# Kernel optimization log

Hardware: AMD Instinct MI355X
Metric: run time of the kernel (lower is better)

## Reference

```python
import jax, jax.numpy as jnp
import numpy as np

D = 1024   # model dim
H = 16     # heads
HD = D // H
L = 14     # layers
FF = 4096  # ffn hidden
T = 768    # sequence length


def layer_norm(x, g, b, eps):
    m = x.mean(-1, keepdims=True)
    v = ((x - m) ** 2).mean(-1, keepdims=True)
    return (x - m) / jnp.sqrt(v + eps) * g + b


def rel_pos_emb(t, d):
    # EspnetRelPositionalEncoding: concat(flip(pe_positive), pe_negative[1:]) -> (1, 2t-1, d)
    pos = jnp.arange(t, dtype=jnp.float32)
    div = jnp.exp(jnp.arange(0, d, 2, dtype=jnp.float32) * (-jnp.log(10000.0) / d))
    ang = pos[:, None] * div[None, :]                              # (t, d/2)
    pe_pos = jnp.stack([jnp.sin(ang), jnp.cos(ang)], -1).reshape(t, d)
    pe_neg = jnp.stack([jnp.sin(-ang), jnp.cos(-ang)], -1).reshape(t, d)
    return jnp.concatenate([pe_pos[::-1], pe_neg[1:]], 0)[None]    # (1, 2t-1, d)


def rel_shift(x):
    # x: (b, h, t, 2t-1) -> (b, h, t, t), Transformer-XL shift
    b, h, t, n = x.shape
    xp = jnp.concatenate([jnp.zeros((b, h, t, 1), x.dtype), x], -1)  # (b,h,t,n+1)
    xp = xp.reshape(b, h, n + 1, t)
    x = xp[:, :, 1:].reshape(b, h, t, n)
    return x[..., : n // 2 + 1]


def setup_inputs() -> dict:
    key = jax.random.key(0)
    ks = iter(jax.random.split(key, 40))
    s = 0.02
    nrm = lambda k, shape: jax.random.normal(k, shape, dtype=jnp.float32) * s
    return {
        "xs": jax.random.normal(next(ks), (1, T, D), dtype=jnp.float32),
        "embed_W": nrm(next(ks), (D, D)), "embed_b": jnp.zeros((D,), jnp.float32),
        "embed_ln_g": jnp.ones((D,), jnp.float32), "embed_ln_b": jnp.zeros((D,), jnp.float32),
        "Wq": nrm(next(ks), (L, D, D)), "bq": jnp.zeros((L, D), jnp.float32),
        "Wk": nrm(next(ks), (L, D, D)), "bk": jnp.zeros((L, D), jnp.float32),
        "Wv": nrm(next(ks), (L, D, D)), "bv": jnp.zeros((L, D), jnp.float32),
        "Wo": nrm(next(ks), (L, D, D)), "bo": jnp.zeros((L, D), jnp.float32),
        "Wp": nrm(next(ks), (L, D, D)),
        "pos_u": nrm(next(ks), (L, H, HD)), "pos_v": nrm(next(ks), (L, H, HD)),
        "ln1_g": jnp.ones((L, D), jnp.float32), "ln1_b": jnp.zeros((L, D), jnp.float32),
        "ln2_g": jnp.ones((L, D), jnp.float32), "ln2_b": jnp.zeros((L, D), jnp.float32),
        "ff_W1": nrm(next(ks), (L, D, FF)), "ff_b1": jnp.zeros((L, FF), jnp.float32),
        "ff_W2": nrm(next(ks), (L, FF, D)), "ff_b2": jnp.zeros((L, D), jnp.float32),
        "after_g": jnp.ones((D,), jnp.float32), "after_b": jnp.zeros((D,), jnp.float32),
    }


def reference(xs, embed_W, embed_b, embed_ln_g, embed_ln_b,
              Wq, bq, Wk, bk, Wv, bv, Wo, bo, Wp, pos_u, pos_v,
              ln1_g, ln1_b, ln2_g, ln2_b, ff_W1, ff_b1, ff_W2, ff_b2,
              after_g, after_b):
    b, t, _ = xs.shape
    # LegacyLinearNoSubsampling: Linear -> LayerNorm(eps=1e-5) -> (dropout) -> ReLU
    h = jnp.maximum(layer_norm(xs @ embed_W + embed_b, embed_ln_g, embed_ln_b, 1e-5), 0.0)
    x = h * jnp.sqrt(jnp.float32(D))          # pos-enc scale factor
    pos = rel_pos_emb(t, D)                    # (1, 2t-1, D)
    scale = jnp.float32(HD) ** -0.5
    for i in range(L):
        res = x
        xn = layer_norm(x, ln1_g[i], ln1_b[i], 1e-12)
        q = (xn @ Wq[i] + bq[i]).reshape(b, t, H, HD).transpose(0, 2, 1, 3)   # bhtd
        k = (xn @ Wk[i] + bk[i]).reshape(b, t, H, HD).transpose(0, 2, 1, 3)
        v = (xn @ Wv[i] + bv[i]).reshape(b, t, H, HD).transpose(0, 2, 1, 3)
        p = (pos @ Wp[i]).reshape(1, 2 * t - 1, H, HD).transpose(0, 2, 1, 3)  # bhnd
        ac = jnp.einsum('bhtd,bhsd->bhts', q + pos_u[i][None, :, None, :], k)
        bd = rel_shift(jnp.einsum('bhtd,bhnd->bhtn', q + pos_v[i][None, :, None, :], p))
        attn = jax.nn.softmax((ac + bd) * scale, axis=-1)
        o = jnp.einsum('bhts,bhsd->bhtd', attn, v).transpose(0, 2, 1, 3).reshape(b, t, D)
        x = res + (o @ Wo[i] + bo[i])
        res = x
        xn = layer_norm(x, ln2_g[i], ln2_b[i], 1e-12)
        x = res + (jnp.maximum(xn @ ff_W1[i] + ff_b1[i], 0.0) @ ff_W2[i] + ff_b2[i])
    return layer_norm(x, after_g, after_b, 1e-5)
```

## Files before the change

### kernel.cpp

```cpp
#include <hip/hip_runtime.h>
#include <hip/hip_bf16.h>
#include <math.h>

#define D_    1024
#define H_    16
#define HD_   64
#define L_    14
#define FF_   4096
#define T_    768
#define NPOS_ (2*T_-1)

using s16x8 = __attribute__((ext_vector_type(8))) short;
using f32x4 = __attribute__((ext_vector_type(4))) float;

__device__ inline short f2bf(float f) {
  __hip_bfloat16 h = __float2bfloat16(f);
  return *reinterpret_cast<short*>(&h);
}
__device__ inline float bf2f(unsigned short u) {
  union { unsigned u; float f; } v; v.u = ((unsigned)u) << 16; return v.f;
}

__device__ inline float waveRedSum(float v) {
#pragma unroll
  for (int o = 32; o > 0; o >>= 1) v += __shfl_down(v, o, 64);
  return v;
}
__device__ inline float blockRedSum(float v, float* sh) {
  int lane = threadIdx.x & 63, wid = threadIdx.x >> 6;
  v = waveRedSum(v);
  if (lane == 0) sh[wid] = v;
  __syncthreads();
  if (wid == 0) {
    float x = (lane < 4) ? sh[lane] : 0.f;
    x = waveRedSum(x);
    if (lane == 0) sh[0] = x;
  }
  __syncthreads();
  float r = sh[0];
  __syncthreads();
  return r;
}

__global__ __launch_bounds__(256) void ln_kernel(
    const float* __restrict__ x, const float* __restrict__ g,
    const float* __restrict__ b, void* __restrict__ y,
    float eps, int relu, float scale, int obf)
{
  __shared__ float sh[8];
  long row = blockIdx.x;
  const float* xr = x + row * D_;
  int tid = threadIdx.x;
  float4 v = *(const float4*)&xr[tid * 4];
  float s  = v.x + v.y + v.z + v.w;
  float sq = v.x * v.x + v.y * v.y + v.z * v.z + v.w * v.w;
  float mean = blockRedSum(s, sh) * (1.f / D_);
  float esq  = blockRedSum(sq, sh) * (1.f / D_);
  float var  = esq - mean * mean;
  if (var < 0.f) var = 0.f;
  float inv = rsqrtf(var + eps);
  float4 gv = *(const float4*)&g[tid * 4];
  float4 bv = *(const float4*)&b[tid * 4];
  float o0 = (v.x - mean) * inv * gv.x + bv.x;
  float o1 = (v.y - mean) * inv * gv.y + bv.y;
  float o2 = (v.z - mean) * inv * gv.z + bv.z;
  float o3 = (v.w - mean) * inv * gv.w + bv.w;
  if (relu) {
    o0 = fmaxf(o0, 0.f); o1 = fmaxf(o1, 0.f);
    o2 = fmaxf(o2, 0.f); o3 = fmaxf(o3, 0.f);
  }
  o0 *= scale; o1 *= scale; o2 *= scale; o3 *= scale;
  if (obf) {
    short4 sv;
    sv.x = f2bf(o0); sv.y = f2bf(o1); sv.z = f2bf(o2); sv.w = f2bf(o3);
    *(short4*)&((unsigned short*)y)[row * D_ + tid * 4] = sv;
  } else {
    float4 ov; ov.x = o0; ov.y = o1; ov.z = o2; ov.w = o3;
    *(float4*)&((float*)y)[row * D_ + tid * 4] = ov;
  }
}

__global__ __launch_bounds__(256) void transpose_kernel(
    const float* __restrict__ in, unsigned short* __restrict__ out, int K, int N)
{
  __shared__ unsigned short t[32][33];
  long z = blockIdx.z;
  in  += z * (long)K * N;
  out += z * (long)K * N;
  int n0 = blockIdx.x * 32, k0 = blockIdx.y * 32;
  int tid = threadIdx.x;
  int r = tid >> 3, c4 = (tid & 7) * 4;
  float4 v = *(const float4*)&in[(long)(k0 + r) * N + n0 + c4];
  t[r][c4 + 0] = (unsigned short)f2bf(v.x);
  t[r][c4 + 1] = (unsigned short)f2bf(v.y);
  t[r][c4 + 2] = (unsigned short)f2bf(v.z);
  t[r][c4 + 3] = (unsigned short)f2bf(v.w);
  __syncthreads();
  ushort4 s;
  s.x = t[c4 + 0][r]; s.y = t[c4 + 1][r]; s.z = t[c4 + 2][r]; s.w = t[c4 + 3][r];
  *(ushort4*)&out[(long)(n0 + r) * K + k0 + c4] = s;
}

template<int BM, int BN, int BMODE, bool CBF16>
__global__ __launch_bounds__(256) void gemm4_kernel(
    const unsigned short* __restrict__ A, int lda, long sAz,
    const void* __restrict__ B0, const void* __restrict__ B1, const void* __restrict__ B2,
    int ldb, long sBz,
    void* C0, void* C1, void* C2, int ldc, long sCz,
    const float* __restrict__ bias0, const float* __restrict__ bias1,
    const float* __restrict__ bias2,
    const float* __restrict__ resid, int ldres,
    int M, int N, int K, int zPerG, int relu, int nM)
{
  constexpr int FM = BM / 32, FN = BN / 32;
  constexpr int A_IT = BM / 32;
  constexpr int NSH = (BN == 128) ? 7 : 6;

  __shared__ short As[BM * 64];
  __shared__ short Bs[BN * 64];

  int nb = gridDim.x, bid = blockIdx.x;
  int q = nb >> 3, r = nb & 7, xcd = bid & 7, idx = bid >> 3;
  int lbid = (xcd < r ? xcd * (q + 1) : r * (q + 1) + (xcd - r) * q) + idx;
  int mT = lbid % nM, nT = lbid / nM;
  int m0 = mT * BM, n0 = nT * BN;

  int z = blockIdx.z;
  int g = z / zPerG, zb = z - g * zPerG;
  A += (long)zb * sAz;
  const void* Bv = (g == 0) ? B0 : ((g == 1) ? B1 : B2);
  void* Cv       = (g == 0) ? C0 : ((g == 1) ? C1 : C2);
  const float* bias = (g == 0) ? bias0 : ((g == 1) ? bias1 : bias2);
  const float* Bf = (const float*)Bv + zb * sBz;
  const unsigned short* Bh = (const unsigned short*)Bv + zb * sBz;
  float* Cf = (float*)Cv + zb * sCz;
  unsigned short* Ch = (unsigned short*)Cv + zb * sCz;

  int tid = threadIdx.x, lane = tid & 63, wid = tid >> 6;
  int wm0 = (wid >> 1) * (BM / 2), wn0 = (wid & 1) * (BN / 2);
  int lr = lane & 15, kl = (lane >> 4) * 8;

  f32x4 acc[FM][FN];
#pragma unroll
  for (int i = 0; i < FM; ++i)
#pragma unroll
    for (int j = 0; j < FN; ++j)
#pragma unroll
      for (int rr = 0; rr < 4; ++rr) acc[i][j][rr] = 0.f;

  for (int k0 = 0; k0 < K; k0 += 64) {
#pragma unroll
    for (int it = 0; it < A_IT; ++it) {
      int f = tid + it * 256;
      int row = f >> 3, c8 = f & 7;
      int gm = m0 + row;
      s16x8 v = {0, 0, 0, 0, 0, 0, 0, 0};
      if (gm < M) v = *(const s16x8*)(A + (long)gm * lda + k0 + c8 * 8);
      *(s16x8*)&As[row * 64 + ((c8 ^ (row & 7)) << 3)] = v;
    }
    if constexpr (BMODE == 1) {
      constexpr int B_IT = BN / 32;
#pragma unroll
      for (int it = 0; it < B_IT; ++it) {
        int f = tid + it * 256;
        int row = f >> 3, c8 = f & 7;
        int gn = n0 + row;
        s16x8 v = *(const s16x8*)(Bh + (long)gn * ldb + k0 + c8 * 8);
        *(s16x8*)&Bs[row * 64 + ((c8 ^ (row & 7)) << 3)] = v;
      }
    } else {
      constexpr int B_IT = BN / 16;
#pragma unroll
      for (int it = 0; it < B_IT; ++it) {
        int p = tid + it * 256;
        int n = p & (BN - 1), kq = p >> NSH;
        int gn = n0 + n;
        const float* bp = Bf + (long)(k0 + kq * 4) * ldb + gn;
        short4 s;
        s.x = f2bf(bp[0]); s.y = f2bf(bp[ldb]);
        s.z = f2bf(bp[2 * (long)ldb]); s.w = f2bf(bp[3 * (long)ldb]);
        *(short4*)&Bs[n * 64 + ((kq << 2) ^ ((n & 7) << 3))] = s;
      }
    }
    __syncthreads();
#pragma unroll
    for (int kk = 0; kk < 2; ++kk) {
      s16x8 a[FM], b[FN];
#pragma unroll
      for (int i = 0; i < FM; ++i) {
        int row = wm0 + i * 16 + lr;
        a[i] = *(const s16x8*)&As[row * 64 + ((kk * 32 + kl) ^ ((lr & 7) << 3))];
      }
#pragma unroll
      for (int j = 0; j < FN; ++j) {
        int row = wn0 + j * 16 + lr;
        b[j] = *(const s16x8*)&Bs[row * 64 + ((kk * 32 + kl) ^ ((lr & 7) << 3))];
      }
#pragma unroll
      for (int i = 0; i < FM; ++i)
#pragma unroll
        for (int j = 0; j < FN; ++j)
          acc[i][j] = __builtin_amdgcn_mfma_f32_16x16x32_bf16(a[i], b[j], acc[i][j], 0, 0, 0);
    }
    __syncthreads();
  }
#pragma unroll
  for (int i = 0; i < FM; ++i) {
#pragma unroll
    for (int j = 0; j < FN; ++j) {
      int n = n0 + wn0 + j * 16 + lr;
      float bv = bias ? bias[n] : 0.f;
#pragma unroll
      for (int rr = 0; rr < 4; ++rr) {
        int m = m0 + wm0 + i * 16 + (lane >> 4) * 4 + rr;
        if (m < M) {
          float v = acc[i][j][rr] + bv;
          if (resid) v += resid[(long)m * ldres + n];
          if (relu)  v = fmaxf(v, 0.f);
          if constexpr (CBF16) Ch[(long)m * ldc + n] = (unsigned short)f2bf(v);
          else                 Cf[(long)m * ldc + n] = v;
        }
      }
    }
  }
}

__global__ __launch_bounds__(256) void f2bf_kernel(
    const float* __restrict__ x, unsigned short* __restrict__ y, int n4)
{
  int i = blockIdx.x * 256 + threadIdx.x;
  if (i >= n4) return;
  float4 v = *(const float4*)&x[i * 4];
  short4 s; s.x = f2bf(v.x); s.y = f2bf(v.y); s.z = f2bf(v.z); s.w = f2bf(v.w);
  *(short4*)&y[i * 4] = s;
}

__global__ __launch_bounds__(256) void pos_kernel(unsigned short* __restrict__ pos)
{
  int idx = blockIdx.x * 256 + threadIdx.x;
  if (idx >= NPOS_ * (D_ / 2)) return;
  int n = idx / (D_ / 2), i = idx % (D_ / 2);
  float r = (float)(T_ - 1 - n);
  float div = __expf((float)(2 * i) * (-logf(10000.f) / (float)D_));
  float ang = r * div;
  pos[(long)n * D_ + 2 * i]     = (unsigned short)f2bf(sinf(ang));
  pos[(long)n * D_ + 2 * i + 1] = (unsigned short)f2bf(cosf(ang));
}

__global__ __launch_bounds__(256) void flash_attn_kernel(
    const unsigned short* __restrict__ Q, const unsigned short* __restrict__ K,
    const unsigned short* __restrict__ V, const unsigned short* __restrict__ P,
    const float* __restrict__ posu, const float* __restrict__ posv,
    unsigned short* __restrict__ O)
{
  __shared__ short Ks[64 * 64];
  __shared__ short Vs[64 * 64];
  __shared__ short Ps[96 * 64];
  __shared__ float Grgn[32 * 99];
  __shared__ float mxls[2][32], smls[2][32];

  short* qu = (short*)Grgn;
  short* qv = qu + 32 * 64;
  float* G  = Grgn;
  short* Pf = (short*)Grgn;

  int h = blockIdx.y;
  int t0 = blockIdx.x * 32;
  int tid = threadIdx.x, lane = tid & 63, w = tid >> 6;
  int wr = w >> 1, wc = w & 1;
  int lr = lane & 15, lg = lane >> 4;
  int kl = lg * 8;
  const float* pu = posu + h * HD_;
  const float* pv = posv + h * HD_;

  {
    int row = tid >> 3, c8 = tid & 7;
    s16x8 q8 = *(const s16x8*)(Q + (long)(t0 + row) * D_ + h * HD_ + c8 * 8);
    const unsigned short* qp = (const unsigned short*)&q8;
    s16x8 su, sv;
#pragma unroll
    for (int j = 0; j < 8; ++j) {
      float qf = bf2f(qp[j]);
      su[j] = f2bf(qf + pu[c8 * 8 + j]);
      sv[j] = f2bf(qf + pv[c8 * 8 + j]);
    }
    int sw = row * 64 + ((c8 ^ (row & 7)) << 3);
    *(s16x8*)&qu[sw] = su;
    *(s16x8*)&qv[sw] = sv;
  }
  __syncthreads();
  s16x8 aqu[2], aqv[2];
#pragma unroll
  for (int kk = 0; kk < 2; ++kk) {
    int row = wr * 16 + lr;
    int col = (kk * 32 + kl) ^ ((lr & 7) << 3);
    aqu[kk] = *(const s16x8*)&qu[row * 64 + col];
    aqv[kk] = *(const s16x8*)&qv[row * 64 + col];
  }

  float m_[4], l_[4];
  f32x4 acc_o[2];
#pragma unroll
  for (int rr = 0; rr < 4; ++rr) { m_[rr] = -1e30f; l_[rr] = 0.f; }
#pragma unroll
  for (int j = 0; j < 2; ++j)
#pragma unroll
    for (int rr = 0; rr < 4; ++rr) acc_o[j][rr] = 0.f;

  for (int s0 = 0; s0 < T_; s0 += 64) {
    int base = s0 - t0 + T_ - 32;
    __syncthreads();
#pragma unroll
    for (int it = 0; it < 2; ++it) {
      int f = tid + it * 256;
      int row = f >> 3, c8 = f & 7;
      s16x8 v = *(const s16x8*)(K + (long)(s0 + row) * D_ + h * HD_ + c8 * 8);
      *(s16x8*)&Ks[row * 64 + ((c8 ^ (row & 7)) << 3)] = v;
    }
#pragma unroll
    for (int it = 0; it < 4; ++it) {
      int d = tid & 63, sq = tid >> 6;
      int s = it * 16 + sq * 4;
      const unsigned short* vp = V + (long)(s0 + s) * D_ + h * HD_ + d;
      short4 sv4;
      sv4.x = (short)vp[0];
      sv4.y = (short)vp[D_];
      sv4.z = (short)vp[2 * D_];
      sv4.w = (short)vp[3 * D_];
      *(short4*)&Vs[d * 64 + (s ^ ((d & 7) << 3))] = sv4;
    }
#pragma unroll
    for (int it = 0; it < 3; ++it) {
      int f = tid + it * 256;
      int row = f >> 3, c8 = f & 7;
      int gp = base + row; if (gp > NPOS_ - 1) gp = NPOS_ - 1;
      s16x8 v = *(const s16x8*)(P + (long)gp * D_ + h * HD_ + c8 * 8);
      *(s16x8*)&Ps[row * 64 + ((c8 ^ (row & 7)) << 3)] = v;
    }
    __syncthreads();
    f32x4 a_ac[2], a_g[3];
#pragma unroll
    for (int j = 0; j < 2; ++j)
#pragma unroll
      for (int rr = 0; rr < 4; ++rr) a_ac[j][rr] = 0.f;
#pragma unroll
    for (int j = 0; j < 3; ++j)
#pragma unroll
      for (int rr = 0; rr < 4; ++rr) a_g[j][rr] = 0.f;
#pragma unroll
    for (int j = 0; j < 2; ++j)
#pragma unroll
      for (int kk = 0; kk < 2; ++kk) {
        int row = wc * 32 + j * 16 + lr;
        s16x8 b = *(const s16x8*)&Ks[row * 64 + ((kk * 32 + kl) ^ ((lr & 7) << 3))];
        a_ac[j] = __builtin_amdgcn_mfma_f32_16x16x32_bf16(aqu[kk], b, a_ac[j], 0, 0, 0);
      }
#pragma unroll
    for (int j = 0; j < 3; ++j)
#pragma unroll
      for (int kk = 0; kk < 2; ++kk) {
        int row = wc * 48 + j * 16 + lr;
        s16x8 b = *(const s16x8*)&Ps[row * 64 + ((kk * 32 + kl) ^ ((lr & 7) << 3))];
        a_g[j] = __builtin_amdgcn_mfma_f32_16x16x32_bf16(aqv[kk], b, a_g[j], 0, 0, 0);
      }
#pragma unroll
    for (int j = 0; j < 3; ++j)
#pragma unroll
      for (int rr = 0; rr < 4; ++rr) {
        int row = wr * 16 + lg * 4 + rr;
        int col = wc * 48 + j * 16 + lr;
        G[row * 99 + col] = a_g[j][rr];
      }
    __syncthreads();
    float sreg[2][4], pm[4];
#pragma unroll
    for (int rr = 0; rr < 4; ++rr) {
      int row = wr * 16 + lg * 4 + rr;
#pragma unroll
      for (int j = 0; j < 2; ++j) {
        int c = wc * 32 + j * 16 + lr;
        int gc = c - row + 31;
        sreg[j][rr] = (a_ac[j][rr] + G[row * 99 + gc]) * 0.125f;
      }
      pm[rr] = fmaxf(sreg[0][rr], sreg[1][rr]);
    }
#pragma unroll
    for (int o = 1; o < 16; o <<= 1)
#pragma unroll
      for (int rr = 0; rr < 4; ++rr) pm[rr] = fmaxf(pm[rr], __shfl_xor(pm[rr], o, 64));
    if (lr == 0) {
#pragma unroll
      for (int rr = 0; rr < 4; ++rr) mxls[wc][wr * 16 + lg * 4 + rr] = pm[rr];
    }
    __syncthreads();
    float ps[4];
#pragma unroll
    for (int rr = 0; rr < 4; ++rr) {
      int row = wr * 16 + lg * 4 + rr;
      float mnew = fmaxf(m_[rr], fmaxf(mxls[0][row], mxls[1][row]));
      float sc = __expf(m_[rr] - mnew);
      m_[rr] = mnew;
      l_[rr] *= sc;
      acc_o[0][rr] *= sc;
      acc_o[1][rr] *= sc;
      float p0 = __expf(sreg[0][rr] - mnew);
      float p1 = __expf(sreg[1][rr] - mnew);
      ps[rr] = p0 + p1;
      int c0 = wc * 32 + lr, c1 = wc * 32 + 16 + lr;
      ((unsigned short*)Pf)[row * 64 + (c0 ^ ((row & 7) << 3))] = (unsigned short)f2bf(p0);
      ((unsigned short*)Pf)[row * 64 + (c1 ^ ((row & 7) << 3))] = (unsigned short)f2bf(p1);
    }
#pragma unroll
    for (int o = 1; o < 16; o <<= 1)
#pragma unroll
      for (int rr = 0; rr < 4; ++rr) ps[rr] += __shfl_xor(ps[rr], o, 64);
    if (lr == 0) {
#pragma unroll
      for (int rr = 0; rr < 4; ++rr) smls[wc][wr * 16 + lg * 4 + rr] = ps[rr];
    }
    __syncthreads();
#pragma unroll
    for (int rr = 0; rr < 4; ++rr) {
      int row = wr * 16 + lg * 4 + rr;
      l_[rr] += smls[0][row] + smls[1][row];
    }
    s16x8 ap[2];
#pragma unroll
    for (int kk = 0; kk < 2; ++kk) {
      int row = wr * 16 + lr;
      ap[kk] = *(const s16x8*)&((unsigned short*)Pf)[row * 64 + ((kk * 32 + kl) ^ ((lr & 7) << 3))];
    }
#pragma unroll
    for (int j = 0; j < 2; ++j)
#pragma unroll
      for (int kk = 0; kk < 2; ++kk) {
        int row = wc * 32 + j * 16 + lr;
        s16x8 b = *(const s16x8*)&Vs[row * 64 + ((kk * 32 + kl) ^ ((lr & 7) << 3))];
        acc_o[j] = __builtin_amdgcn_mfma_f32_16x16x32_bf16(ap[kk], b, acc_o[j], 0, 0, 0);
      }
  }
#pragma unroll
  for (int j = 0; j < 2; ++j)
#pragma unroll
    for (int rr = 0; rr < 4; ++rr) {
      int row = t0 + wr * 16 + lg * 4 + rr;
      int col = h * HD_ + wc * 32 + j * 16 + lr;
      O[(long)row * D_ + col] = (unsigned short)f2bf(acc_o[j][rr] / l_[rr]);
    }
}

extern "C" void kernel_launch(void* const* d_in, const int* in_sizes, int n_in,
                              void* d_out, int out_size, void* d_ws, size_t ws_size,
                              hipStream_t stream) {
  const float* xs       = (const float*)d_in[0];
  const float* embed_W  = (const float*)d_in[1];
  const float* embed_b  = (const float*)d_in[2];
  const float* embed_g  = (const float*)d_in[3];
  const float* embed_bt = (const float*)d_in[4];
  const float* Wq = (const float*)d_in[5];
  const float* bq = (const float*)d_in[6];
  const float* Wk = (const float*)d_in[7];
  const float* bk = (const float*)d_in[8];
  const float* Wv = (const float*)d_in[9];
  const float* bv = (const float*)d_in[10];
  const float* Wo = (const float*)d_in[11];
  const float* bo = (const float*)d_in[12];
  const float* Wp = (const float*)d_in[13];
  const float* pos_u = (const float*)d_in[14];
  const float* pos_v = (const float*)d_in[15];
  const float* ln1_g = (const float*)d_in[16];
  const float* ln1_b = (const float*)d_in[17];
  const float* ln2_g = (const float*)d_in[18];
  const float* ln2_b = (const float*)d_in[19];
  const float* ff_W1 = (const float*)d_in[20];
  const float* ff_b1 = (const float*)d_in[21];
  const float* ff_W2 = (const float*)d_in[22];
  const float* ff_b2 = (const float*)d_in[23];
  const float* after_g = (const float*)d_in[24];
  const float* after_b = (const float*)d_in[25];
  float* out = (float*)d_out;

  char* w = (char*)d_ws;
  auto carve = [&](size_t bytes) { char* p = w; w += (bytes + 255) & ~(size_t)255; return p; };
  float* bufX  = (float*)carve((size_t)T_ * D_ * 4);
  float* bufT  = (float*)carve((size_t)T_ * D_ * 4);
  unsigned short* xsb  = (unsigned short*)carve((size_t)T_ * D_ * 2);
  unsigned short* XNb  = (unsigned short*)carve((size_t)T_ * D_ * 2);
  unsigned short* Qb   = (unsigned short*)carve((size_t)T_ * D_ * 2);
  unsigned short* Kb   = (unsigned short*)carve((size_t)T_ * D_ * 2);
  unsigned short* Vb   = (unsigned short*)carve((size_t)T_ * D_ * 2);
  unsigned short* Ob   = (unsigned short*)carve((size_t)T_ * D_ * 2);
  unsigned short* Hb   = (unsigned short*)carve((size_t)T_ * FF_ * 2);
  unsigned short* posT = (unsigned short*)carve((size_t)NPOS_ * D_ * 2);
  unsigned short* Pall = (unsigned short*)carve((size_t)L_ * NPOS_ * D_ * 2);
  size_t szDD = (size_t)D_ * D_;
  unsigned short* embedWt = (unsigned short*)carve(szDD * 2);
  unsigned short* WqT = (unsigned short*)carve((size_t)L_ * szDD * 2);
  unsigned short* WkT = (unsigned short*)carve((size_t)L_ * szDD * 2);
  unsigned short* WvT = (unsigned short*)carve((size_t)L_ * szDD * 2);
  unsigned short* WoT = (unsigned short*)carve((size_t)L_ * szDD * 2);
  unsigned short* WpT = (unsigned short*)carve((size_t)L_ * szDD * 2);
  unsigned short* W1T = (unsigned short*)carve((size_t)L_ * D_ * FF_ * 2);
  unsigned short* W2T = (unsigned short*)carve((size_t)L_ * D_ * FF_ * 2);
  bool fast = ((size_t)(w - (char*)d_ws) <= ws_size);

  {
    int n = NPOS_ * (D_ / 2);
    pos_kernel<<<(n + 255) / 256, 256, 0, stream>>>(posT);
  }
  f2bf_kernel<<<(T_ * D_ / 4 + 255) / 256, 256, 0, stream>>>(xs, xsb, T_ * D_ / 4);

  if (fast) {
    transpose_kernel<<<dim3(32, 32, 1),  256, 0, stream>>>(embed_W, embedWt, D_, D_);
    transpose_kernel<<<dim3(32, 32, L_), 256, 0, stream>>>(Wq, WqT, D_, D_);
    transpose_kernel<<<dim3(32, 32, L_), 256, 0, stream>>>(Wk, WkT, D_, D_);
    transpose_kernel<<<dim3(32, 32, L_), 256, 0, stream>>>(Wv, WvT, D_, D_);
    transpose_kernel<<<dim3(32, 32, L_), 256, 0, stream>>>(Wo, WoT, D_, D_);
    transpose_kernel<<<dim3(32, 32, L_), 256, 0, stream>>>(Wp, WpT, D_, D_);
    transpose_kernel<<<dim3(128, 32, L_), 256, 0, stream>>>(ff_W1, W1T, D_, FF_);
    transpose_kernel<<<dim3(32, 128, L_), 256, 0, stream>>>(ff_W2, W2T, FF_, D_);

    gemm4_kernel<32, 128, 1, false><<<dim3(192, 1, 1), 256, 0, stream>>>(
        xsb, D_, 0, embedWt, nullptr, nullptr, D_, 0,
        bufT, nullptr, nullptr, D_, 0, embed_b, nullptr, nullptr,
        nullptr, 0, T_, D_, D_, 1, 0, 24);
    ln_kernel<<<T_, 256, 0, stream>>>(bufT, embed_g, embed_bt, bufX, 1e-5f, 1, 32.0f, 0);

    gemm4_kernel<128, 64, 1, true><<<dim3(192, 1, 14), 256, 0, stream>>>(
        posT, D_, 0, WpT, nullptr, nullptr, D_, (long)szDD,
        Pall, nullptr, nullptr, D_, (long)NPOS_ * D_, nullptr, nullptr, nullptr,
        nullptr, 0, NPOS_, D_, D_, 14, 0, 12);

    for (int i = 0; i < L_; ++i) {
      ln_kernel<<<T_, 256, 0, stream>>>(bufX, ln1_g + (long)i * D_, ln1_b + (long)i * D_,
                                        XNb, 1e-12f, 0, 1.0f, 1);
      gemm4_kernel<32, 128, 1, true><<<dim3(192, 1, 3), 256, 0, stream>>>(
          XNb, D_, 0, WqT + i * szDD, WkT + i * szDD, WvT + i * szDD, D_, 0,
          Qb, Kb, Vb, D_, 0,
          bq + (long)i * D_, bk + (long)i * D_, bv + (long)i * D_,
          nullptr, 0, T_, D_, D_, 1, 0, 24);
      flash_attn_kernel<<<dim3(T_ / 32, H_), 256, 0, stream>>>(
          Qb, Kb, Vb, Pall + (long)i * NPOS_ * D_,
          pos_u + (long)i * D_, pos_v + (long)i * D_, Ob);
      gemm4_kernel<32, 64, 1, false><<<dim3(384, 1, 1), 256, 0, stream>>>(
          Ob, D_, 0, WoT + i * szDD, nullptr, nullptr, D_, 0,
          bufX, nullptr, nullptr, D_, 0, bo + (long)i * D_, nullptr, nullptr,
          bufX, D_, T_, D_, D_, 1, 0, 24);
      ln_kernel<<<T_, 256, 0, stream>>>(bufX, ln2_g + (long)i * D_, ln2_b + (long)i * D_,
                                        XNb, 1e-12f, 0, 1.0f, 1);
      gemm4_kernel<32, 128, 1, true><<<dim3(768, 1, 1), 256, 0, stream>>>(
          XNb, D_, 0, W1T + (size_t)i * D_ * FF_, nullptr, nullptr, D_, 0,
          Hb, nullptr, nullptr, FF_, 0, ff_b1 + (long)i * FF_, nullptr, nullptr,
          nullptr, 0, T_, FF_, D_, 1, 1, 24);
      gemm4_kernel<32, 64, 1, false><<<dim3(384, 1, 1), 256, 0, stream>>>(
          Hb, FF_, 0, W2T + (size_t)i * D_ * FF_, nullptr, nullptr, FF_, 0,
          bufX, nullptr, nullptr, D_, 0, ff_b2 + (long)i * D_, nullptr, nullptr,
          bufX, D_, T_, FF_, FF_, 1, 0, 24);
    }
  } else {
    gemm4_kernel<32, 128, 0, false><<<dim3(192, 1, 1), 256, 0, stream>>>(
        xsb, D_, 0, embed_W, nullptr, nullptr, D_, 0,
        bufT, nullptr, nullptr, D_, 0, embed_b, nullptr, nullptr,
        nullptr, 0, T_, D_, D_, 1, 0, 24);
    ln_kernel<<<T_, 256, 0, stream>>>(bufT, embed_g, embed_bt, bufX, 1e-5f, 1, 32.0f, 0);

    gemm4_kernel<128, 64, 0, true><<<dim3(192, 1, 14), 256, 0, stream>>>(
        posT, D_, 0, Wp, nullptr, nullptr, D_, (long)szDD,
        Pall, nullptr, nullptr, D_, (long)NPOS_ * D_, nullptr, nullptr, nullptr,
        nullptr, 0, NPOS_, D_, D_, 14, 0, 12);

    for (int i = 0; i < L_; ++i) {
      ln_kernel<<<T_, 256, 0, stream>>>(bufX, ln1_g + (long)i * D_, ln1_b + (long)i * D_,
                                        XNb, 1e-12f, 0, 1.0f, 1);
      gemm4_kernel<32, 128, 0, true><<<dim3(192, 1, 3), 256, 0, stream>>>(
          XNb, D_, 0, Wq + i * szDD, Wk + i * szDD, Wv + i * szDD, D_, 0,
          Qb, Kb, Vb, D_, 0,
          bq + (long)i * D_, bk + (long)i * D_, bv + (long)i * D_,
          nullptr, 0, T_, D_, D_, 1, 0, 24);
      flash_attn_kernel<<<dim3(T_ / 32, H_), 256, 0, stream>>>(
          Qb, Kb, Vb, Pall + (long)i * NPOS_ * D_,
          pos_u + (long)i * D_, pos_v + (long)i * D_, Ob);
      gemm4_kernel<32, 64, 0, false><<<dim3(384, 1, 1), 256, 0, stream>>>(
          Ob, D_, 0, Wo + i * szDD, nullptr, nullptr, D_, 0,
          bufX, nullptr, nullptr, D_, 0, bo + (long)i * D_, nullptr, nullptr,
          bufX, D_, T_, D_, D_, 1, 0, 24);
      ln_kernel<<<T_, 256, 0, stream>>>(bufX, ln2_g + (long)i * D_, ln2_b + (long)i * D_,
                                        XNb, 1e-12f, 0, 1.0f, 1);
      gemm4_kernel<32, 128, 0, true><<<dim3(768, 1, 1), 256, 0, stream>>>(
          XNb, D_, 0, ff_W1 + (size_t)i * D_ * FF_, nullptr, nullptr, FF_, 0,
          Hb, nullptr, nullptr, FF_, 0, ff_b1 + (long)i * FF_, nullptr, nullptr,
          nullptr, 0, T_, FF_, D_, 1, 1, 24);
      gemm4_kernel<32, 64, 0, false><<<dim3(384, 1, 1), 256, 0, stream>>>(
          Hb, FF_, 0, ff_W2 + (size_t)i * D_ * FF_, nullptr, nullptr, D_, 0,
          bufX, nullptr, nullptr, D_, 0, ff_b2 + (long)i * D_, nullptr, nullptr,
          bufX, D_, T_, FF_, FF_, 1, 0, 24);
    }
  }

  ln_kernel<<<T_, 256, 0, stream>>>(bufX, after_g, after_b, out, 1e-5f, 0, 1.0f, 0);
}
```

Baseline: 2.501 ms.

## Add 32x32x16 MFMA GEMM kernel with configurable wave layout for fast path

After: 3.029 ms. 1.21x slower.

```diff
diff --git a/kernel.cpp b/kernel.cpp
--- a/kernel.cpp
+++ b/kernel.cpp
@@ -10,8 +10,9 @@
 #define T_    768
 #define NPOS_ (2*T_-1)
 
-using s16x8 = __attribute__((ext_vector_type(8))) short;
-using f32x4 = __attribute__((ext_vector_type(4))) float;
+using s16x8  = __attribute__((ext_vector_type(8))) short;
+using f32x4  = __attribute__((ext_vector_type(4))) float;
+using f32x16 = __attribute__((ext_vector_type(16))) float;
 
 __device__ inline short f2bf(float f) {
   __hip_bfloat16 h = __float2bfloat16(f);
@@ -101,8 +102,103 @@
   *(ushort4*)&out[(long)(n0 + r) * K + k0 + c4] = s;
 }
 
-template<int BM, int BN, int BMODE, bool CBF16>
-__global__ __launch_bounds__(256) void gemm4_kernel(
+template<int BM, int BN, int WM, int WN, bool CBF16>
+__global__ __launch_bounds__(WM * WN * 64) void gemm7_kernel(
+    const unsigned short* __restrict__ A, int lda, long sAz,
+    const unsigned short* __restrict__ B0, const unsigned short* __restrict__ B1,
+    const unsigned short* __restrict__ B2, int ldb, long sBz,
+    void* C0, void* C1, void* C2, int ldc, long sCz,
+    const float* __restrict__ bias0, const float* __restrict__ bias1,
+    const float* __restrict__ bias2,
+    const float* __restrict__ resid, int ldres,
+    int M, int N, int K, int zPerG, int relu, int nM)
+{
+  constexpr int NT = WM * WN * 64;
+  constexpr int FM = BM / WM / 32;
+  constexpr int A_IT = BM * 8 / NT;
+  constexpr int B_IT = BN * 8 / NT;
+
+  __shared__ short As[BM * 64];
+  __shared__ short Bs[BN * 64];
+
+  int nb = gridDim.x, bid = blockIdx.x;
+  int q = nb >> 3, r = nb & 7, xcd = bid & 7, idx = bid >> 3;
+  int lbid = (xcd < r ? xcd * (q + 1) : r * (q + 1) + (xcd - r) * q) + idx;
+  int mT = lbid % nM, nT = lbid / nM;
+  int m0 = mT * BM, n0 = nT * BN;
+
+  int z = blockIdx.z;
+  int g = z / zPerG, zb = z - g * zPerG;
+  A += (long)zb * sAz;
+  const unsigned short* Bh = ((g == 0) ? B0 : ((g == 1) ? B1 : B2)) + zb * sBz;
+  void* Cv = (g == 0) ? C0 : ((g == 1) ? C1 : C2);
+  const float* bias = (g == 0) ? bias0 : ((g == 1) ? bias1 : bias2);
+  float* Cf = (float*)Cv + zb * sCz;
+  unsigned short* Ch = (unsigned short*)Cv + zb * sCz;
+
+  int tid = threadIdx.x, lane = tid & 63, wid = tid >> 6;
+  int wrow = wid / WN, wcol = wid % WN;
+  int wm0 = wrow * (BM / WM), wn0 = wcol * 32;
+  int l31 = lane & 31, khalf = lane >> 5;
+
+  f32x16 acc[FM];
+#pragma unroll
+  for (int i = 0; i < FM; ++i)
+#pragma unroll
+    for (int rr = 0; rr < 16; ++rr) acc[i][rr] = 0.f;
+
+  for (int k0 = 0; k0 < K; k0 += 64) {
+#pragma unroll
+    for (int it = 0; it < A_IT; ++it) {
+      int f = tid + it * NT;
+      int row = f >> 3, c8 = f & 7;
+      int gm = m0 + row;
+      s16x8 v = {0, 0, 0, 0, 0, 0, 0, 0};
+      if (gm < M) v = *(const s16x8*)(A + (long)gm * lda + k0 + c8 * 8);
+      *(s16x8*)&As[row * 64 + ((c8 ^ (row & 7)) << 3)] = v;
+    }
+#pragma unroll
+    for (int it = 0; it < B_IT; ++it) {
+      int f = tid + it * NT;
+      int row = f >> 3, c8 = f & 7;
+      s16x8 v = *(const s16x8*)(Bh + (long)(n0 + row) * ldb + k0 + c8 * 8);
+      *(s16x8*)&Bs[row * 64 + ((c8 ^ (row & 7)) << 3)] = v;
+    }
+    __syncthreads();
+#pragma unroll
+    for (int ks = 0; ks < 4; ++ks) {
+      int c8 = ks * 2 + khalf;
+      int nrow = wn0 + l31;
+      s16x8 b = *(const s16x8*)&Bs[nrow * 64 + ((c8 ^ (nrow & 7)) << 3)];
+#pragma unroll
+      for (int i = 0; i < FM; ++i) {
+        int mrow = wm0 + i * 32 + l31;
+        s16x8 a = *(const s16x8*)&As[mrow * 64 + ((c8 ^ (mrow & 7)) << 3)];
+        acc[i] = __builtin_amdgcn_mfma_f32_32x32x16_bf16(a, b, acc[i], 0, 0, 0);
+      }
+    }
+    __syncthreads();
+  }
+  int n = n0 + wn0 + l31;
+  float bv = bias ? bias[n] : 0.f;
+#pragma unroll
+  for (int i = 0; i < FM; ++i) {
+#pragma unroll
+    for (int reg = 0; reg < 16; ++reg) {
+      int m = m0 + wm0 + i * 32 + (reg & 3) + 8 * (reg >> 2) + 4 * khalf;
+      if (m < M) {
+        float v = acc[i][reg] + bv;
+        if (resid) v += resid[(long)m * ldres + n];
+        if (relu)  v = fmaxf(v, 0.f);
+        if constexpr (CBF16) Ch[(long)m * ldc + n] = (unsigned short)f2bf(v);
+        else                 Cf[(long)m * ldc + n] = v;
+      }
+    }
+  }
+}
+
+template<int BM, int BN, bool CBF16>
+__global__ __launch_bounds__(256) void gemm5_kernel(
     const unsigned short* __restrict__ A, int lda, long sAz,
     const void* __restrict__ B0, const void* __restrict__ B1, const void* __restrict__ B2,
     int ldb, long sBz,
@@ -132,7 +228,6 @@
   void* Cv       = (g == 0) ? C0 : ((g == 1) ? C1 : C2);
   const float* bias = (g == 0) ? bias0 : ((g == 1) ? bias1 : bias2);
   const float* Bf = (const float*)Bv + zb * sBz;
-  const unsigned short* Bh = (const unsigned short*)Bv + zb * sBz;
   float* Cf = (float*)Cv + zb * sCz;
   unsigned short* Ch = (unsigned short*)Cv + zb * sCz;
 
@@ -158,29 +253,17 @@
       if (gm < M) v = *(const s16x8*)(A + (long)gm * lda + k0 + c8 * 8);
       *(s16x8*)&As[row * 64 + ((c8 ^ (row & 7)) << 3)] = v;
     }
-    if constexpr (BMODE == 1) {
-      constexpr int B_IT = BN / 32;
-#pragma unroll
-      for (int it = 0; it < B_IT; ++it) {
-        int f = tid + it * 256;
-        int row = f >> 3, c8 = f & 7;
-        int gn = n0 + row;
-        s16x8 v = *(const s16x8*)(Bh + (long)gn * ldb + k0 + c8 * 8);
-        *(s16x8*)&Bs[row * 64 + ((c8 ^ (row & 7)) << 3)] = v;
-      }
-    } else {
-      constexpr int B_IT = BN / 16;
-#pragma unroll
-      for (int it = 0; it < B_IT; ++it) {
-        int p = tid + it * 256;
-        int n = p & (BN - 1), kq = p >> NSH;
-        int gn = n0 + n;
-        const float* bp = Bf + (long)(k0 + kq * 4) * ldb + gn;
-        short4 s;
-        s.x = f2bf(bp[0]); s.y = f2bf(bp[ldb]);
-        s.z = f2bf(bp[2 * (long)ldb]); s.w = f2bf(bp[3 * (long)ldb]);
-        *(short4*)&Bs[n * 64 + ((kq << 2) ^ ((n & 7) << 3))] = s;
-      }
+    constexpr int B_IT2 = BN / 16;
+#pragma unroll
+    for (int it = 0; it < B_IT2; ++it) {
+      int p = tid + it * 256;
+      int n = p & (BN - 1), kq = p >> NSH;
+      int gn = n0 + n;
+      const float* bp = Bf + (long)(k0 + kq * 4) * ldb + gn;
+      short4 s;
+      s.x = f2bf(bp[0]); s.y = f2bf(bp[ldb]);
+      s.z = f2bf(bp[2 * (long)ldb]); s.w = f2bf(bp[3 * (long)ldb]);
+      *(short4*)&Bs[n * 64 + ((kq << 2) ^ ((n & 7) << 3))] = s;
     }
     __syncthreads();
 #pragma unroll
@@ -491,7 +574,7 @@
   unsigned short* Vb   = (unsigned short*)carve((size_t)T_ * D_ * 2);
   unsigned short* Ob   = (unsigned short*)carve((size_t)T_ * D_ * 2);
   unsigned short* Hb   = (unsigned short*)carve((size_t)T_ * FF_ * 2);
-  unsigned short* posT = (unsigned short*)carve((size_t)NPOS_ * D_ * 2);
+  unsigned short* posT = (unsigned short*)carve((size_t)(NPOS_ + 16) * D_ * 2);
   unsigned short* Pall = (unsigned short*)carve((size_t)L_ * NPOS_ * D_ * 2);
   size_t szDD = (size_t)D_ * D_;
   unsigned short* embedWt = (unsigned short*)carve(szDD * 2);
@@ -520,13 +603,13 @@
     transpose_kernel<<<dim3(128, 32, L_), 256, 0, stream>>>(ff_W1, W1T, D_, FF_);
     transpose_kernel<<<dim3(32, 128, L_), 256, 0, stream>>>(ff_W2, W2T, FF_, D_);
 
-    gemm4_kernel<32, 128, 1, false><<<dim3(192, 1, 1), 256, 0, stream>>>(
+    gemm7_kernel<32, 128, 1, 4, false><<<dim3(192, 1, 1), 256, 0, stream>>>(
         xsb, D_, 0, embedWt, nullptr, nullptr, D_, 0,
         bufT, nullptr, nullptr, D_, 0, embed_b, nullptr, nullptr,
         nullptr, 0, T_, D_, D_, 1, 0, 24);
     ln_kernel<<<T_, 256, 0, stream>>>(bufT, embed_g, embed_bt, bufX, 1e-5f, 1, 32.0f, 0);
 
-    gemm4_kernel<128, 64, 1, true><<<dim3(192, 1, 14), 256, 0, stream>>>(
+    gemm7_kernel<128, 64, 2, 2, true><<<dim3(192, 1, 14), 256, 0, stream>>>(
         posT, D_, 0, WpT, nullptr, nullptr, D_, (long)szDD,
         Pall, nullptr, nullptr, D_, (long)NPOS_ * D_, nullptr, nullptr, nullptr,
         nullptr, 0, NPOS_, D_, D_, 14, 0, 12);
@@ -534,7 +617,7 @@
     for (int i = 0; i < L_; ++i) {
       ln_kernel<<<T_, 256, 0, stream>>>(bufX, ln1_g + (long)i * D_, ln1_b + (long)i * D_,
                                         XNb, 1e-12f, 0, 1.0f, 1);
-      gemm4_kernel<32, 128, 1, true><<<dim3(192, 1, 3), 256, 0, stream>>>(
+      gemm7_kernel<32, 128, 1, 4, true><<<dim3(192, 1, 3), 256, 0, stream>>>(
           XNb, D_, 0, WqT + i * szDD, WkT + i * szDD, WvT + i * szDD, D_, 0,
           Qb, Kb, Vb, D_, 0,
           bq + (long)i * D_, bk + (long)i * D_, bv + (long)i * D_,
@@ -542,29 +625,29 @@
       flash_attn_kernel<<<dim3(T_ / 32, H_), 256, 0, stream>>>(
           Qb, Kb, Vb, Pall + (long)i * NPOS_ * D_,
           pos_u + (long)i * D_, pos_v + (long)i * D_, Ob);
-      gemm4_kernel<32, 64, 1, false><<<dim3(384, 1, 1), 256, 0, stream>>>(
+      gemm7_kernel<32, 64, 1, 2, false><<<dim3(384, 1, 1), 128, 0, stream>>>(
           Ob, D_, 0, WoT + i * szDD, nullptr, nullptr, D_, 0,
           bufX, nullptr, nullptr, D_, 0, bo + (long)i * D_, nullptr, nullptr,
           bufX, D_, T_, D_, D_, 1, 0, 24);
       ln_kernel<<<T_, 256, 0, stream>>>(bufX, ln2_g + (long)i * D_, ln2_b + (long)i * D_,
                                         XNb, 1e-12f, 0, 1.0f, 1);
-      gemm4_kernel<32, 128, 1, true><<<dim3(768, 1, 1), 256, 0, stream>>>(
+      gemm7_kernel<32, 128, 1, 4, true><<<dim3(768, 1, 1), 256, 0, stream>>>(
           XNb, D_, 0, W1T + (size_t)i * D_ * FF_, nullptr, nullptr, D_, 0,
           Hb, nullptr, nullptr, FF_, 0, ff_b1 + (long)i * FF_, nullptr, nullptr,
           nullptr, 0, T_, FF_, D_, 1, 1, 24);
-      gemm4_kernel<32, 64, 1, false><<<dim3(384, 1, 1), 256, 0, stream>>>(
+      gemm7_kernel<32, 64, 1, 2, false><<<dim3(384, 1, 1), 128, 0, stream>>>(
           Hb, FF_, 0, W2T + (size_t)i * D_ * FF_, nullptr, nullptr, FF_, 0,
           bufX, nullptr, nullptr, D_, 0, ff_b2 + (long)i * D_, nullptr, nullptr,
           bufX, D_, T_, FF_, FF_, 1, 0, 24);
     }
   } else {
-    gemm4_kernel<32, 128, 0, false><<<dim3(192, 1, 1), 256, 0, stream>>>(
+    gemm5_kernel<32, 128, false><<<dim3(192, 1, 1), 256, 0, stream>>>(
         xsb, D_, 0, embed_W, nullptr, nullptr, D_, 0,
         bufT, nullptr, nullptr, D_, 0, embed_b, nullptr, nullptr,
         nullptr, 0, T_, D_, D_, 1, 0, 24);
     ln_kernel<<<T_, 256, 0, stream>>>(bufT, embed_g, embed_bt, bufX, 1e-5f, 1, 32.0f, 0);
 
-    gemm4_kernel<128, 64, 0, true><<<dim3(192, 1, 14), 256, 0, stream>>>(
+    gemm5_kernel<128, 64, true><<<dim3(192, 1, 14), 256, 0, stream>>>(
         posT, D_, 0, Wp, nullptr, nullptr, D_, (long)szDD,
         Pall, nullptr, nullptr, D_, (long)NPOS_ * D_, nullptr, nullptr, nullptr,
         nullptr, 0, NPOS_, D_, D_, 14, 0, 12);
@@ -572,7 +655,7 @@
     for (int i = 0; i < L_; ++i) {
       ln_kernel<<<T_, 256, 0, stream>>>(bufX, ln1_g + (long)i * D_, ln1_b + (long)i * D_,
                                         XNb, 1e-12f, 0, 1.0f, 1);
-      gemm4_kernel<32, 128, 0, true><<<dim3(192, 1, 3), 256, 0, stream>>>(
+      gemm5_kernel<32, 128, true><<<dim3(192, 1, 3), 256, 0, stream>>>(
           XNb, D_, 0, Wq + i * szDD, Wk + i * szDD, Wv + i * szDD, D_, 0,
           Qb, Kb, Vb, D_, 0,
           bq + (long)i * D_, bk + (long)i * D_, bv + (long)i * D_,
@@ -580,17 +663,17 @@
       flash_attn_kernel<<<dim3(T_ / 32, H_), 256, 0, stream>>>(
           Qb, Kb, Vb, Pall + (long)i * NPOS_ * D_,
           pos_u + (long)i * D_, pos_v + (long)i * D_, Ob);
-      gemm4_kernel<32, 64, 0, false><<<dim3(384, 1, 1), 256, 0, stream>>>(
+      gemm5_kernel<32, 64, false><<<dim3(384, 1, 1), 256, 0, stream>>>(
           Ob, D_, 0, Wo + i * szDD, nullptr, nullptr, D_, 0,
           bufX, nullptr, nullptr, D_, 0, bo + (long)i * D_, nullptr, nullptr,
           bufX, D_, T_, D_, D_, 1, 0, 24);
       ln_kernel<<<T_, 256, 0, stream>>>(bufX, ln2_g + (long)i * D_, ln2_b + (long)i * D_,
                                         XNb, 1e-12f, 0, 1.0f, 1);
-      gemm4_kernel<32, 128, 0, true><<<dim3(768, 1, 1), 256, 0, stream>>>(
+      gemm5_kernel<32, 128, true><<<dim3(768, 1, 1), 256, 0, stream>>>(
           XNb, D_, 0, ff_W1 + (size_t)i * D_ * FF_, nullptr, nullptr, FF_, 0,
           Hb, nullptr, nullptr, FF_, 0, ff_b1 + (long)i * FF_, nullptr, nullptr,
           nullptr, 0, T_, FF_, D_, 1, 1, 24);
-      gemm4_kernel<32, 64, 0, false><<<dim3(384, 1, 1), 256, 0, stream>>>(
+      gemm5_kernel<32, 64, false><<<dim3(384, 1, 1), 256, 0, stream>>>(
           Hb, FF_, 0, ff_W2 + (size_t)i * D_ * FF_, nullptr, nullptr, D_, 0,
           bufX, nullptr, nullptr, D_, 0, ff_b2 + (long)i * D_, nullptr, nullptr,
           bufX, D_, T_, FF_, FF_, 1, 0, 24);
```
